# Kernel optimization log

Measured on AMD Instinct MI355X. Metric: run time of the kernel, lower is better.

Reference implementation:

```python
import jax, jax.numpy as jnp
import numpy as np

B, N, D, L, K, H = 64, 576, 768, 64, 5, 8  # batch, tokens, dim, out_token_len, knn k, heads
HD = D // H
SCALE = HD ** -0.5


def layer_norm(x, g, b, eps=1e-5):
    m = jnp.mean(x, axis=-1, keepdims=True)
    v = jnp.mean((x - m) ** 2, axis=-1, keepdims=True)
    return (x - m) * jax.lax.rsqrt(v + eps) * g + b


def cluster(feat, noise):
    # DPC-KNN: pairwise distances, k-NN density, parent distance, peak selection
    sq = jnp.sum(feat * feat, axis=-1)  # [B,N]
    dm = sq[:, :, None] + sq[:, None, :] - 2.0 * jnp.einsum('bnd,bmd->bnm', feat, feat)
    dm = jnp.sqrt(jnp.maximum(dm, 0.0)) / jnp.sqrt(jnp.asarray(D, feat.dtype))  # [B,N,N]
    neg_near, _ = jax.lax.top_k(-dm, K)                       # k smallest distances (negated)
    density = jnp.exp(-jnp.mean(neg_near ** 2, axis=-1))      # [B,N]
    density = density + noise * 1e-6                          # deterministic tie-break
    mask = (density[:, None, :] > density[:, :, None]).astype(feat.dtype)
    dist_max = jnp.max(dm.reshape(dm.shape[0], -1), axis=-1)[:, None, None]
    dist = jnp.min(dm * mask + dist_max * (1.0 - mask), axis=-1)  # [B,N]
    score = dist * density
    _, idx_down = jax.lax.top_k(score, L)                     # [B,L] cluster centers
    dm_down = jnp.take_along_axis(dm, idx_down[:, :, None], axis=1)  # [B,L,N]
    idx_cluster = jnp.argmin(dm_down, axis=1)                 # [B,N] assign to nearest center
    idx_cluster = idx_cluster.at[jnp.arange(dm.shape[0])[:, None], idx_down].set(
        jnp.arange(L)[None, :])
    return idx_cluster


def merger(feat, idx_cluster, token_score):
    b, n, d = feat.shape
    idx = (idx_cluster + jnp.arange(b)[:, None] * L).reshape(-1)       # [B*N]
    tw = jnp.exp(token_score)                                          # [B,N,1]
    all_w = jax.ops.segment_sum(tw.reshape(-1, 1), idx, num_segments=b * L) + 1e-6
    norm_w = tw / all_w[idx].reshape(b, n, 1)
    merged = jax.ops.segment_sum((feat * norm_w).reshape(-1, d), idx, num_segments=b * L)
    return merged.reshape(b, L, d)


def setup_inputs() -> dict:
    key = jax.random.key(0)
    ks = jax.random.split(key, 16)
    s = 0.02
    return {
        'x': jax.random.normal(ks[0], (B, N, D), jnp.float32),
        'density_noise': jax.random.uniform(ks[1], (B, N), jnp.float32),
        'norm1_g': jnp.ones((D,), jnp.float32),
        'norm1_b': jnp.zeros((D,), jnp.float32),
        'score_w': s * jax.random.normal(ks[2], (D, 1), jnp.float32),
        'score_b': jnp.zeros((1,), jnp.float32),
        'wq': s * jax.random.normal(ks[3], (D, D), jnp.float32),
        'wk': s * jax.random.normal(ks[4], (D, D), jnp.float32),
        'wv': s * jax.random.normal(ks[5], (D, D), jnp.float32),
        'proj_w': s * jax.random.normal(ks[6], (D, D), jnp.float32),
        'proj_b': jnp.zeros((D,), jnp.float32),
        'norm2_g': jnp.ones((D,), jnp.float32),
        'norm2_b': jnp.zeros((D,), jnp.float32),
        'fc1_w': s * jax.random.normal(ks[7], (D, 4 * D), jnp.float32),
        'fc1_b': jnp.zeros((4 * D,), jnp.float32),
        'fc2_w': s * jax.random.normal(ks[8], (4 * D, D), jnp.float32),
        'fc2_b': jnp.zeros((D,), jnp.float32),
    }


def reference(x, density_noise, norm1_g, norm1_b, score_w, score_b, wq, wk, wv,
              proj_w, proj_b, norm2_g, norm2_b, fc1_w, fc1_b, fc2_w, fc2_b):
    xn = layer_norm(x, norm1_g, norm1_b)                 # [B,N,D]
    token_score = xn @ score_w + score_b                 # [B,N,1]
    idx_cluster = cluster(jax.lax.stop_gradient(xn), density_noise)  # no-grad in torch
    q_input = merger(xn, idx_cluster, token_score)       # [B,L,D]
    kv = xn
    # STMAttention: cross-attn with token_score bias added to logits
    q = (q_input @ wq).reshape(B, L, H, HD).transpose(0, 2, 1, 3)
    k = (kv @ wk).reshape(B, N, H, HD).transpose(0, 2, 1, 3)
    v = (kv @ wv).reshape(B, N, H, HD).transpose(0, 2, 1, 3)
    dots = jnp.einsum('bhid,bhjd->bhij', q, k) * SCALE   # [B,H,L,N]
    bias = token_score[:, :, 0][:, None, None, :]        # [B,1,1,N]
    attn = jax.nn.softmax(dots + bias, axis=-1)
    out = jnp.einsum('bhij,bhjd->bhid', attn, v)
    out = out.transpose(0, 2, 1, 3).reshape(B, L, D)
    out = out @ proj_w + proj_b
    feature = q_input + out
    h = layer_norm(feature, norm2_g, norm2_b)
    h = jax.nn.gelu(h @ fc1_w + fc1_b, approximate=False) @ fc2_w + fc2_b
    return feature + h
```

## Files before the change

kernel.cpp:

```cpp
#include <hip/hip_runtime.h>
#include <math.h>

#define B_   64
#define N_   576
#define D_   768
#define L_   64
#define H_   8
#define HD_  96
#define NB_  (B_*N_)
#define ML_  (B_*L_)
#define KV_STRIDE_ 1536
#define SCALE_ 0.10206207f
#define INV_SQRT_D_ 0.03608439182f
#define LO_SCALE_ 4.8828125e-4f

typedef __attribute__((ext_vector_type(8))) _Float16 half8v;
typedef __attribute__((ext_vector_type(4))) float floatx4;

__device__ __forceinline__ unsigned short f2h(float f) {
  _Float16 h = (_Float16)f;
  unsigned short u; __builtin_memcpy(&u, &h, 2);
  return u;
}
__device__ __forceinline__ float h2f(unsigned short u) {
  _Float16 h; __builtin_memcpy(&h, &u, 2);
  return (float)h;
}
__device__ __forceinline__ void gload_lds16(const void* g, void* l) {
  __builtin_amdgcn_global_load_lds(
      (const __attribute__((address_space(1))) unsigned*)g,
      (__attribute__((address_space(3))) unsigned*)l, 16, 0, 0);
}

__global__ __launch_bounds__(256) void k_ln1(const float* __restrict__ x,
    const float* __restrict__ g, const float* __restrict__ bt,
    const float* __restrict__ sw, const float* __restrict__ sb,
    unsigned short* __restrict__ xh, unsigned short* __restrict__ xl,
    float* __restrict__ ts, float* __restrict__ sq)
{
  int row = blockIdx.x, tid = threadIdx.x;
  const float* xr = x + (size_t)row * D_;
  float v0 = xr[tid], v1 = xr[tid + 256], v2 = xr[tid + 512];
  __shared__ float r1[256], r2[256];
  r1[tid] = v0 + v1 + v2;
  r2[tid] = v0 * v0 + v1 * v1 + v2 * v2;
  __syncthreads();
  for (int o = 128; o > 0; o >>= 1) {
    if (tid < o) { r1[tid] += r1[tid + o]; r2[tid] += r2[tid + o]; }
    __syncthreads();
  }
  float mean = r1[0] * (1.0f / D_);
  float var  = r2[0] * (1.0f / D_) - mean * mean;
  float rstd = rsqrtf(var + 1e-5f);
  __syncthreads();
  float o0 = (v0 - mean) * rstd * g[tid      ] + bt[tid      ];
  float o1 = (v1 - mean) * rstd * g[tid + 256] + bt[tid + 256];
  float o2 = (v2 - mean) * rstd * g[tid + 512] + bt[tid + 512];
  auto split = [](float o, unsigned short& hu, unsigned short& lu) {
    _Float16 h = (_Float16)o;
    float hf = (float)h;
    _Float16 l = (_Float16)((o - hf) * 2048.0f);
    __builtin_memcpy(&hu, &h, 2);
    __builtin_memcpy(&lu, &l, 2);
  };
  unsigned short h0, l0, h1, l1, h2, l2;
  split(o0, h0, l0); split(o1, h1, l1); split(o2, h2, l2);
  unsigned short* xho = xh + (size_t)row * D_;
  unsigned short* xlo = xl + (size_t)row * D_;
  xho[tid] = h0; xho[tid + 256] = h1; xho[tid + 512] = h2;
  xlo[tid] = l0; xlo[tid + 256] = l1; xlo[tid + 512] = l2;
  r1[tid] = o0 * sw[tid] + o1 * sw[tid + 256] + o2 * sw[tid + 512];
  r2[tid] = o0 * o0 + o1 * o1 + o2 * o2;
  __syncthreads();
  for (int o = 128; o > 0; o >>= 1) {
    if (tid < o) { r1[tid] += r1[tid + o]; r2[tid] += r2[tid + o]; }
    __syncthreads();
  }
  if (tid == 0) { ts[row] = r1[0] + sb[0]; sq[row] = r2[0]; }
}

__global__ __launch_bounds__(256) void k_dmg(const unsigned short* __restrict__ xh,
    const unsigned short* __restrict__ xl, const float* __restrict__ sq,
    float* __restrict__ dm, float* __restrict__ dmax)
{
  __shared__ __align__(16) unsigned short S[4][96 * 64];
  int flat = blockIdx.x;
  int xcd = flat & 7, seq = flat >> 3;
  int b = (seq / 21) * 8 + xcd;
  int t = seq % 21;
  int ti = 0, rl = 6;
  while (t >= rl) { t -= rl; ++ti; --rl; }
  int tj = ti + t;
  int tid = threadIdx.x;
  int wave = tid >> 6, lane = tid & 63;
  int wr = (wave >> 1) * 48, wc = (wave & 1) * 48;
  int mloc = lane & 15, quad = lane >> 4;
  size_t rowA = (size_t)b * N_ + ti * 96;
  size_t rowB = (size_t)b * N_ + tj * 96;

  const unsigned short* srcbase =
      (wave == 0) ? xh + rowA * D_ :
      (wave == 1) ? xl + rowA * D_ :
      (wave == 2) ? xh + rowB * D_ : xl + rowB * D_;
  int lrow = lane >> 3, lchunk = lane & 7;
  const unsigned short* gsrc0 = srcbase + (size_t)lrow * D_ + ((lchunk ^ lrow) * 8);
  unsigned short* lbase = &S[wave][0];

  floatx4 a1[3][3], a2[3][3];
#pragma unroll
  for (int i = 0; i < 3; ++i)
#pragma unroll
    for (int j = 0; j < 3; ++j) {
      a1[i][j] = (floatx4){0.f, 0.f, 0.f, 0.f};
      a2[i][j] = (floatx4){0.f, 0.f, 0.f, 0.f};
    }

  for (int kt = 0; kt < D_; kt += 64) {
    __syncthreads();
#pragma unroll
    for (int rb = 0; rb < 12; ++rb)
      gload_lds16(gsrc0 + (size_t)rb * 8 * D_ + kt, lbase + rb * 8 * 64);
    __syncthreads();
#pragma unroll
    for (int ks = 0; ks < 2; ++ks) {
      half8v ah[3], al[3], bh[3], bl[3];
      int cperm = (((ks << 2) | quad) ^ (mloc & 7)) * 8;
#pragma unroll
      for (int i = 0; i < 3; ++i) {
        int ro = (wr + i * 16 + mloc) * 64 + cperm;
        ah[i] = *(const half8v*)&S[0][ro];
        al[i] = *(const half8v*)&S[1][ro];
      }
#pragma unroll
      for (int j = 0; j < 3; ++j) {
        int ro = (wc + j * 16 + mloc) * 64 + cperm;
        bh[j] = *(const half8v*)&S[2][ro];
        bl[j] = *(const half8v*)&S[3][ro];
      }
#pragma unroll
      for (int i = 0; i < 3; ++i)
#pragma unroll
        for (int j = 0; j < 3; ++j) {
          a1[i][j] = __builtin_amdgcn_mfma_f32_16x16x32_f16(ah[i], bh[j], a1[i][j], 0, 0, 0);
          a2[i][j] = __builtin_amdgcn_mfma_f32_16x16x32_f16(ah[i], bl[j], a2[i][j], 0, 0, 0);
          a2[i][j] = __builtin_amdgcn_mfma_f32_16x16x32_f16(al[i], bh[j], a2[i][j], 0, 0, 0);
        }
    }
  }

  const float* sqb = sq + b * N_;
  float* dmb = dm + (size_t)b * N_ * N_;
  bool diag = (ti == tj);
  float vmax = 0.f;
#pragma unroll
  for (int j = 0; j < 3; ++j) {
    int gj = tj * 96 + wc + j * 16 + mloc;
    float sj = sqb[gj];
#pragma unroll
    for (int i = 0; i < 3; ++i) {
      int gi0 = ti * 96 + wr + i * 16 + quad * 4;
#pragma unroll
      for (int reg = 0; reg < 4; ++reg) {
        int gi = gi0 + reg;
        float g = a1[i][j][reg] + a2[i][j][reg] * LO_SCALE_;
        float d = sqb[gi] + sj - 2.0f * g;
        float v = sqrtf(fmaxf(d, 0.0f)) * INV_SQRT_D_;
        vmax = fmaxf(vmax, v);
        if (!diag || gj >= gi) {
          dmb[(size_t)gi * N_ + gj] = v;
          dmb[(size_t)gj * N_ + gi] = v;
        }
      }
    }
  }
#pragma unroll
  for (int msk = 32; msk >= 1; msk >>= 1) vmax = fmaxf(vmax, __shfl_xor(vmax, msk));
  if (lane == 0) atomicMax((unsigned int*)(dmax + b), __float_as_uint(vmax));
}

__global__ __launch_bounds__(64) void k_density(const float* __restrict__ dm,
    const float* __restrict__ noise, float* __restrict__ den)
{
  int row = blockIdx.x, lane = threadIdx.x;
  const float* r = dm + (size_t)row * N_;
  float a0 = 1e30f, a1 = 1e30f, a2 = 1e30f, a3 = 1e30f, a4 = 1e30f;
  auto ins5 = [&](float xv) {
    a4 = fminf(a4, xv);
    float t;
    t = fminf(a3, a4); a4 = fmaxf(a3, a4); a3 = t;
    t = fminf(a2, a3); a3 = fmaxf(a2, a3); a2 = t;
    t = fminf(a1, a2); a2 = fmaxf(a1, a2); a1 = t;
    t = fminf(a0, a1); a1 = fmaxf(a0, a1); a0 = t;
  };
#pragma unroll
  for (int t = 0; t < 9; ++t) ins5(r[lane + 64 * t]);
  for (int m = 1; m < 64; m <<= 1) {
    float b0 = __shfl_xor(a0, m), b1 = __shfl_xor(a1, m), b2 = __shfl_xor(a2, m);
    float b3 = __shfl_xor(a3, m), b4 = __shfl_xor(a4, m);
    ins5(b0); ins5(b1); ins5(b2); ins5(b3); ins5(b4);
  }
  if (lane == 0) {
    float ms = (a0 * a0 + a1 * a1 + a2 * a2 + a3 * a3 + a4 * a4) * 0.2f;
    den[row] = expf(-ms) + noise[row] * 1e-6f;
  }
}

__global__ __launch_bounds__(64) void k_dist(const float* __restrict__ dm,
    const float* __restrict__ den, const float* __restrict__ dmax,
    float* __restrict__ score)
{
  int row = blockIdx.x, lane = threadIdx.x;
  int b = row / N_;
  float di = den[row], dx = dmax[b];
  const float* r = dm + (size_t)row * N_;
  const float* db = den + b * N_;
  float m = dx;
#pragma unroll
  for (int t = 0; t < 9; ++t) {
    int j = lane + 64 * t;
    float v = (db[j] > di) ? r[j] : dx;
    m = fminf(m, v);
  }
  for (int msk = 1; msk < 64; msk <<= 1) m = fminf(m, __shfl_xor(m, msk));
  if (lane == 0) score[row] = m * di;
}

__global__ __launch_bounds__(256) void k_topL(const float* __restrict__ score,
    int* __restrict__ idxd)
{
  int b = blockIdx.x, tid = threadIdx.x;
  __shared__ float s[1024];
  __shared__ int   si[1024];
  for (int i = tid; i < 1024; i += 256) {
    s[i] = (i < N_) ? score[b * N_ + i] : -3.0e38f;
    si[i] = i;
  }
  __syncthreads();
  for (int k = 2; k <= 1024; k <<= 1) {
    for (int j = k >> 1; j > 0; j >>= 1) {
#pragma unroll
      for (int t = 0; t < 2; ++t) {
        int idx512 = tid + t * 256;
        int lo = idx512 & (j - 1);
        int i = ((idx512 ^ lo) << 1) | lo;
        int p = i | j;
        float as = s[i], bs = s[p];
        int ai = si[i], bi = si[p];
        bool bba = (bs > as) || (bs == as && bi < ai);
        bool up = ((i & k) == 0);
        bool dosw = up ? bba : !bba;
        if (dosw) { s[i] = bs; s[p] = as; si[i] = bi; si[p] = ai; }
      }
      __syncthreads();
    }
  }
  if (tid < L_) idxd[b * L_ + tid] = si[tid];
}

__global__ __launch_bounds__(576) void k_assign(const float* __restrict__ dm,
    const int* __restrict__ idxd, int* __restrict__ idxc)
{
  int b = blockIdx.x, n = threadIdx.x;
  __shared__ int ctr[L_];
  if (n < L_) ctr[n] = idxd[b * L_ + n];
  __syncthreads();
  const float* dmb = dm + (size_t)b * N_ * N_;
  float best = 1e30f; int bl = 0;
  for (int l = 0; l < L_; ++l) {
    float v = dmb[(size_t)ctr[l] * N_ + n];
    if (v < best) { best = v; bl = l; }
  }
  for (int l = 0; l < L_; ++l)
    if (ctr[l] == n) bl = l;
  idxc[b * N_ + n] = bl;
}

__global__ __launch_bounds__(64) void k_bucket(const int* __restrict__ idxc,
    int* __restrict__ ord, int* __restrict__ starts)
{
  int b = blockIdx.x, l = threadIdx.x;
  __shared__ int ic[N_];
  for (int n = l; n < N_; n += 64) ic[n] = idxc[b * N_ + n];
  __syncthreads();
  int cnt = 0;
  for (int n = 0; n < N_; ++n) cnt += (ic[n] == l) ? 1 : 0;
  int inc = cnt;
  for (int d = 1; d < 64; d <<= 1) {
    int v = __shfl_up(inc, d);
    if (l >= d) inc += v;
  }
  int excl = inc - cnt;
  if (l == 0) starts[b * 65] = 0;
  starts[b * 65 + l + 1] = inc;
  int p = excl;
  for (int n = 0; n < N_; ++n)
    if (ic[n] == l) ord[b * N_ + p++] = n;
}

__global__ __launch_bounds__(256) void k_merge(const unsigned short* __restrict__ xh,
    const unsigned short* __restrict__ xl,
    const float* __restrict__ ts, const int* __restrict__ ord,
    const int* __restrict__ starts, float* __restrict__ qin)
{
  int blk = blockIdx.x;
  int b = blk >> 6, l = blk & 63;
  int tid = threadIdx.x;
  int s0 = starts[b * 65 + l], s1 = starts[b * 65 + l + 1];
  const float* tsb = ts + b * N_;
  const int* ob = ord + b * N_;
  const unsigned short* xhb = xh + (size_t)b * N_ * D_;
  const unsigned short* xlb = xl + (size_t)b * N_ * D_;
  float a0 = 0.f, a1 = 0.f, a2 = 0.f, wsum = 0.f;
  for (int k = s0; k < s1; ++k) {
    int n = ob[k];
    float w = expf(tsb[n]);
    wsum += w;
    const unsigned short* hr = xhb + (size_t)n * D_;
    const unsigned short* lr = xlb + (size_t)n * D_;
    float x0 = h2f(hr[tid      ]) + h2f(lr[tid      ]) * LO_SCALE_;
    float x1 = h2f(hr[tid + 256]) + h2f(lr[tid + 256]) * LO_SCALE_;
    float x2 = h2f(hr[tid + 512]) + h2f(lr[tid + 512]) * LO_SCALE_;
    a0 += w * x0; a1 += w * x1; a2 += w * x2;
  }
  float inv = 1.0f / (wsum + 1e-6f);
  float* q = qin + (size_t)blk * D_;
  q[tid] = a0 * inv; q[tid + 256] = a1 * inv; q[tid + 512] = a2 * inv;
}

__global__ __launch_bounds__(256) void k_wt(const float* __restrict__ W,
    unsigned short* __restrict__ WT, int K, int N)
{
  __shared__ float t[32][33];
  int k0 = blockIdx.x * 32, n0 = blockIdx.y * 32;
  int tid = threadIdx.x;
  int r = tid >> 3, c4 = (tid & 7) * 4;
  float4 v = *(const float4*)(W + (size_t)(k0 + r) * N + n0 + c4);
  t[r][c4] = v.x; t[r][c4 + 1] = v.y; t[r][c4 + 2] = v.z; t[r][c4 + 3] = v.w;
  __syncthreads();
  ushort4 s4;
  s4.x = f2h(t[c4 + 0][r]); s4.y = f2h(t[c4 + 1][r]);
  s4.z = f2h(t[c4 + 2][r]); s4.w = f2h(t[c4 + 3][r]);
  *(ushort4*)(WT + (size_t)(n0 + r) * K + k0 + c4) = s4;
}

template<int EPI, int ASRC>
__global__ __launch_bounds__(256) void k_mgemm(const void* __restrict__ Ap_,
    const unsigned short* __restrict__ Wt, const float* __restrict__ bias,
    const float* __restrict__ res, void* __restrict__ outp,
    int M, int Nd, int Kd)
{
  __shared__ __align__(16) unsigned short As[128 * 64];
  __shared__ __align__(16) unsigned short Bs[128 * 64];
  int tid = threadIdx.x;
  int gn = Nd >> 7;
  int flat = blockIdx.x;
  int xcd = flat & 7, seq = flat >> 3;
  int bmg = seq / gn, bnn = seq - bmg * gn;
  int bm = (bmg * 8 + xcd) * 128, bn = bnn * 128;
  int wave = tid >> 6, lane = tid & 63;
  int wr = (wave >> 1) * 64, wc = (wave & 1) * 64;
  int mloc = lane & 15, quad = lane >> 4;

  floatx4 acc[4][4];
#pragma unroll
  for (int i = 0; i < 4; ++i)
#pragma unroll
    for (int j = 0; j < 4; ++j)
      acc[i][j] = (floatx4){0.f, 0.f, 0.f, 0.f};

  int lrow = lane >> 3, lchunk = lane & 7;
  const unsigned short* bsrc0 =
      Wt + (size_t)(bn + wave * 32 + lrow) * Kd + ((lchunk ^ lrow) * 8);
  unsigned short* bdst0 = &Bs[(wave * 32) * 64];
  const unsigned short* asrc0 = (ASRC == 1)
      ? (const unsigned short*)Ap_ + (size_t)(bm + wave * 32 + lrow) * Kd + ((lchunk ^ lrow) * 8)
      : nullptr;
  unsigned short* adst0 = &As[(wave * 32) * 64];

  for (int kt = 0; kt < Kd; kt += 64) {
    __syncthreads();
#pragma unroll
    for (int rb = 0; rb < 4; ++rb)
      gload_lds16(bsrc0 + (size_t)rb * 8 * Kd + kt, bdst0 + rb * 8 * 64);
    if (ASRC == 1) {
#pragma unroll
      for (int rb = 0; rb < 4; ++rb)
        gload_lds16(asrc0 + (size_t)rb * 8 * Kd + kt, adst0 + rb * 8 * 64);
    } else {
      const float* A = (const float*)Ap_;
#pragma unroll
      for (int it = 0; it < 4; ++it) {
        int idx = tid + it * 256;
        int r = idx >> 3, c = idx & 7;
        const float* ap = A + (size_t)(bm + r) * Kd + kt + c * 8;
        float4 f0 = *(const float4*)ap;
        float4 f1 = *(const float4*)(ap + 4);
        uint4 pk;
        pk.x = (unsigned)f2h(f0.x) | ((unsigned)f2h(f0.y) << 16);
        pk.y = (unsigned)f2h(f0.z) | ((unsigned)f2h(f0.w) << 16);
        pk.z = (unsigned)f2h(f1.x) | ((unsigned)f2h(f1.y) << 16);
        pk.w = (unsigned)f2h(f1.z) | ((unsigned)f2h(f1.w) << 16);
        *(uint4*)&As[r * 64 + ((c ^ (r & 7)) * 8)] = pk;
      }
    }
    __syncthreads();
#pragma unroll
    for (int ks = 0; ks < 2; ++ks) {
      half8v af[4], bf[4];
      int cperm = (((ks << 2) | quad) ^ (mloc & 7)) * 8;
#pragma unroll
      for (int i = 0; i < 4; ++i)
        af[i] = *(const half8v*)&As[(wr + i * 16 + mloc) * 64 + cperm];
#pragma unroll
      for (int j = 0; j < 4; ++j)
        bf[j] = *(const half8v*)&Bs[(wc + j * 16 + mloc) * 64 + cperm];
#pragma unroll
      for (int i = 0; i < 4; ++i)
#pragma unroll
        for (int j = 0; j < 4; ++j)
          acc[i][j] = __builtin_amdgcn_mfma_f32_16x16x32_f16(af[i], bf[j], acc[i][j], 0, 0, 0);
    }
  }

  float bv[4] = {0.f, 0.f, 0.f, 0.f};
  if (EPI >= 1) {
#pragma unroll
    for (int j = 0; j < 4; ++j) bv[j] = bias[bn + wc + j * 16 + mloc];
  }
#pragma unroll
  for (int i = 0; i < 4; ++i) {
    int gr0 = bm + wr + i * 16 + quad * 4;
#pragma unroll
    for (int j = 0; j < 4; ++j) {
      int gcn = bn + wc + j * 16 + mloc;
#pragma unroll
      for (int reg = 0; reg < 4; ++reg) {
        float v = acc[i][j][reg];
        size_t off = (size_t)(gr0 + reg) * Nd + gcn;
        if (EPI == 0) {
          ((unsigned short*)outp)[off] = f2h(v);
        } else if (EPI == 1) {
          ((float*)outp)[off] = v + bv[j] + res[off];
        } else {
          v += bv[j];
          v = 0.5f * v * (1.0f + erff(v * 0.70710678f));
          ((unsigned short*)outp)[off] = f2h(v);
        }
      }
    }
  }
}

__global__ __launch_bounds__(256) void k_attn(const unsigned short* __restrict__ Qu,
    const unsigned short* __restrict__ KVu, const float* __restrict__ ts,
    float* __restrict__ aout)
{
  __shared__ __align__(16) unsigned short Ks[64 * 104];
  __shared__ __align__(16) unsigned short VsT[96 * 64];
  __shared__ __align__(16) unsigned short sPa[64 * 64];
  __shared__ float tsb[64];
  int h = blockIdx.x, b = blockIdx.y;
  int tid = threadIdx.x;
  int wave = tid >> 6, lane = tid & 63;
  int mloc = lane & 15, quad = lane >> 4;

  half8v qf[3];
  {
    const unsigned short* qrow = Qu + (size_t)(b * 64 + wave * 16 + mloc) * D_ + h * 96 + quad * 8;
#pragma unroll
    for (int k = 0; k < 3; ++k) qf[k] = *(const half8v*)(qrow + k * 32);
  }

  floatx4 of[6];
#pragma unroll
  for (int dt = 0; dt < 6; ++dt) of[dt] = (floatx4){0.f, 0.f, 0.f, 0.f};
  float m[4], l[4];
#pragma unroll
  for (int r = 0; r < 4; ++r) { m[r] = -1e30f; l[r] = 0.f; }

  for (int jt = 0; jt < 9; ++jt) {
    int j0 = jt * 64;
    __syncthreads();
#pragma unroll
    for (int t = 0; t < 3; ++t) {
      int id = tid + t * 256;
      int row = id / 12, c = id % 12;
      *(uint4*)&Ks[row * 104 + c * 8] =
          *(const uint4*)(KVu + (size_t)(b * N_ + j0 + row) * KV_STRIDE_ + h * 96 + c * 8);
    }
#pragma unroll
    for (int t = 0; t < 3; ++t) {
      int id = tid + t * 256;
      int keyp = id & 31, dq = (id >> 5) * 4;
      int key = keyp * 2;
      const unsigned short* vp =
          KVu + (size_t)(b * N_ + j0 + key) * KV_STRIDE_ + 768 + h * 96 + dq;
      ushort4 v0 = *(const ushort4*)vp;
      ushort4 v1 = *(const ushort4*)(vp + KV_STRIDE_);
      unsigned pk0 = (unsigned)v0.x | ((unsigned)v1.x << 16);
      unsigned pk1 = (unsigned)v0.y | ((unsigned)v1.y << 16);
      unsigned pk2 = (unsigned)v0.z | ((unsigned)v1.z << 16);
      unsigned pk3 = (unsigned)v0.w | ((unsigned)v1.w << 16);
      int cbase = key >> 3, off = key & 7;
#pragma unroll
      for (int i = 0; i < 4; ++i) {
        int d = dq + i;
        unsigned pv = (i == 0) ? pk0 : (i == 1) ? pk1 : (i == 2) ? pk2 : pk3;
        *(unsigned*)&VsT[d * 64 + ((cbase ^ (d & 7)) << 3) + off] = pv;
      }
    }
    if (tid < 64) tsb[tid] = ts[b * N_ + j0 + tid];
    __syncthreads();

    floatx4 acc[4];
#pragma unroll
    for (int j = 0; j < 4; ++j) acc[j] = (floatx4){0.f, 0.f, 0.f, 0.f};
#pragma unroll
    for (int j = 0; j < 4; ++j)
#pragma unroll
      for (int k = 0; k < 3; ++k) {
        half8v kf = *(const half8v*)&Ks[(j * 16 + mloc) * 104 + k * 32 + quad * 8];
        acc[j] = __builtin_amdgcn_mfma_f32_16x16x32_f16(qf[k], kf, acc[j], 0, 0, 0);
      }

    float ts4[4];
#pragma unroll
    for (int j = 0; j < 4; ++j) ts4[j] = tsb[j * 16 + mloc];
    float rm[4] = {-1e30f, -1e30f, -1e30f, -1e30f};
#pragma unroll
    for (int j = 0; j < 4; ++j)
#pragma unroll
      for (int r = 0; r < 4; ++r) {
        acc[j][r] = acc[j][r] * SCALE_ + ts4[j];
        rm[r] = fmaxf(rm[r], acc[j][r]);
      }
#pragma unroll
    for (int r = 0; r < 4; ++r) {
      rm[r] = fmaxf(rm[r], __shfl_xor(rm[r], 1));
      rm[r] = fmaxf(rm[r], __shfl_xor(rm[r], 2));
      rm[r] = fmaxf(rm[r], __shfl_xor(rm[r], 4));
      rm[r] = fmaxf(rm[r], __shfl_xor(rm[r], 8));
    }
    float alpha[4], rs[4];
#pragma unroll
    for (int r = 0; r < 4; ++r) {
      float mn = fmaxf(m[r], rm[r]);
      alpha[r] = __expf(m[r] - mn);
      m[r] = mn;
      rs[r] = 0.f;
    }
#pragma unroll
    for (int j = 0; j < 4; ++j)
#pragma unroll
      for (int r = 0; r < 4; ++r) {
        float p = __expf(acc[j][r] - m[r]);
        acc[j][r] = p; rs[r] += p;
      }
#pragma unroll
    for (int r = 0; r < 4; ++r) {
      rs[r] += __shfl_xor(rs[r], 1); rs[r] += __shfl_xor(rs[r], 2);
      rs[r] += __shfl_xor(rs[r], 4); rs[r] += __shfl_xor(rs[r], 8);
      l[r] = l[r] * alpha[r] + rs[r];
    }
#pragma unroll
    for (int dt = 0; dt < 6; ++dt)
#pragma unroll
      for (int r = 0; r < 4; ++r) of[dt][r] *= alpha[r];

#pragma unroll
    for (int j = 0; j < 4; ++j)
#pragma unroll
      for (int r = 0; r < 4; ++r) {
        int row = wave * 16 + quad * 4 + r;
        int key = j * 16 + mloc;
        sPa[row * 64 + (((key >> 3) ^ (row & 7)) << 3) + (key & 7)] = f2h(acc[j][r]);
      }
    half8v pa[2];
    int prow = wave * 16 + mloc;
#pragma unroll
    for (int f2 = 0; f2 < 2; ++f2)
      pa[f2] = *(const half8v*)&sPa[prow * 64 + (((f2 * 4 + quad) ^ (prow & 7)) << 3)];
#pragma unroll
    for (int dt = 0; dt < 6; ++dt)
#pragma unroll
      for (int f2 = 0; f2 < 2; ++f2) {
        int vrow = dt * 16 + mloc;
        half8v vf = *(const half8v*)&VsT[vrow * 64 + (((f2 * 4 + quad) ^ (vrow & 7)) << 3)];
        of[dt] = __builtin_amdgcn_mfma_f32_16x16x32_f16(pa[f2], vf, of[dt], 0, 0, 0);
      }
  }

  float linv[4];
#pragma unroll
  for (int r = 0; r < 4; ++r) linv[r] = 1.0f / l[r];
#pragma unroll
  for (int dt = 0; dt < 6; ++dt)
#pragma unroll
    for (int r = 0; r < 4; ++r) {
      int row = b * 64 + wave * 16 + quad * 4 + r;
      int col = h * 96 + dt * 16 + mloc;
      aout[(size_t)row * D_ + col] = of[dt][r] * linv[r];
    }
}

__global__ __launch_bounds__(256) void k_ln2(const float* __restrict__ f,
    const float* __restrict__ g, const float* __restrict__ bt, float* __restrict__ out)
{
  int row = blockIdx.x, tid = threadIdx.x;
  const float* fr = f + (size_t)row * D_;
  float v0 = fr[tid], v1 = fr[tid + 256], v2 = fr[tid + 512];
  __shared__ float r1[256], r2[256];
  r1[tid] = v0 + v1 + v2;
  r2[tid] = v0 * v0 + v1 * v1 + v2 * v2;
  __syncthreads();
  for (int o = 128; o > 0; o >>= 1) {
    if (tid < o) { r1[tid] += r1[tid + o]; r2[tid] += r2[tid + o]; }
    __syncthreads();
  }
  float mean = r1[0] * (1.0f / D_);
  float var  = r2[0] * (1.0f / D_) - mean * mean;
  float rstd = rsqrtf(var + 1e-5f);
  float* oo = out + (size_t)row * D_;
  oo[tid      ] = (v0 - mean) * rstd * g[tid      ] + bt[tid      ];
  oo[tid + 256] = (v1 - mean) * rstd * g[tid + 256] + bt[tid + 256];
  oo[tid + 512] = (v2 - mean) * rstd * g[tid + 512] + bt[tid + 512];
}

extern "C" void kernel_launch(void* const* d_in, const int* in_sizes, int n_in,
                              void* d_out, int out_size, void* d_ws, size_t ws_size,
                              hipStream_t stream)
{
  (void)in_sizes; (void)n_in; (void)out_size; (void)ws_size;
  const float* x    = (const float*)d_in[0];
  const float* nois = (const float*)d_in[1];
  const float* n1g  = (const float*)d_in[2];
  const float* n1b  = (const float*)d_in[3];
  const float* sw   = (const float*)d_in[4];
  const float* sb   = (const float*)d_in[5];
  const float* wq   = (const float*)d_in[6];
  const float* wk   = (const float*)d_in[7];
  const float* wv   = (const float*)d_in[8];
  const float* pw   = (const float*)d_in[9];
  const float* pb   = (const float*)d_in[10];
  const float* n2g  = (const float*)d_in[11];
  const float* n2b  = (const float*)d_in[12];
  const float* f1w  = (const float*)d_in[13];
  const float* f1b  = (const float*)d_in[14];
  const float* f2w  = (const float*)d_in[15];
  const float* f2b  = (const float*)d_in[16];

  float* ws    = (float*)d_ws;
  unsigned short* XH = (unsigned short*)ws;
  unsigned short* XL = XH + (size_t)NB_ * D_;
  float* RG    = ws + (size_t)NB_ * D_;
  float* QIN   = RG + (size_t)NB_ * D_;
  float* FEAT  = QIN + (size_t)ML_ * D_;
  float* AOUT  = FEAT + (size_t)ML_ * D_;
  float* QBUF  = AOUT + (size_t)ML_ * D_;
  float* P     = QBUF + (size_t)ML_ * D_;
  unsigned short* QH16 = (unsigned short*)P;  P += (size_t)ML_ * D_ / 2;
  unsigned short* WTQ  = (unsigned short*)P;  P += (size_t)D_ * D_ / 2;
  unsigned short* WTKV = (unsigned short*)P;  P += (size_t)D_ * D_;
  unsigned short* WTP  = (unsigned short*)P;  P += (size_t)D_ * D_ / 2;
  unsigned short* WT1  = (unsigned short*)P;  P += (size_t)D_ * 4 * D_ / 2;
  unsigned short* WT2  = (unsigned short*)P;  P += (size_t)D_ * 4 * D_ / 2;
  float* TS    = P;
  float* SQ    = TS + NB_;
  float* DEN   = SQ + NB_;
  float* SCORE = DEN + NB_;
  float* DMAX  = SCORE + NB_;
  int*   IDXD  = (int*)(DMAX + 64);
  int*   IDXC  = IDXD + ML_;
  int*   ORD   = IDXC + NB_;
  int*   STARTS= ORD + NB_;
  float* DM    = RG;
  unsigned short* KVB = (unsigned short*)RG;
  unsigned short* HID = (unsigned short*)RG;

  hipMemsetAsync(DMAX, 0, 64 * sizeof(float), stream);
  k_wt<<<dim3(24, 24), 256, 0, stream>>>(wq, WTQ, D_, D_);
  k_wt<<<dim3(24, 24), 256, 0, stream>>>(wk, WTKV, D_, D_);
  k_wt<<<dim3(24, 24), 256, 0, stream>>>(wv, WTKV + (size_t)D_ * D_, D_, D_);
  k_wt<<<dim3(24, 24), 256, 0, stream>>>(pw, WTP, D_, D_);
  k_wt<<<dim3(24, 96), 256, 0, stream>>>(f1w, WT1, D_, 4 * D_);
  k_wt<<<dim3(96, 24), 256, 0, stream>>>(f2w, WT2, 4 * D_, D_);

  k_ln1<<<NB_, 256, 0, stream>>>(x, n1g, n1b, sw, sb, XH, XL, TS, SQ);
  k_dmg<<<1344, 256, 0, stream>>>(XH, XL, SQ, DM, DMAX);
  k_density<<<NB_, 64, 0, stream>>>(DM, nois, DEN);
  k_dist<<<NB_, 64, 0, stream>>>(DM, DEN, DMAX, SCORE);
  k_topL<<<B_, 256, 0, stream>>>(SCORE, IDXD);
  k_assign<<<B_, 576, 0, stream>>>(DM, IDXD, IDXC);
  k_bucket<<<B_, 64, 0, stream>>>(IDXC, ORD, STARTS);
  k_merge<<<ML_, 256, 0, stream>>>(XH, XL, TS, ORD, STARTS, QIN);

  k_mgemm<0, 0><<<(ML_ / 128) * (D_ / 128), 256, 0, stream>>>(
      QIN, WTQ, nullptr, nullptr, QH16, ML_, D_, D_);
  k_mgemm<0, 1><<<(NB_ / 128) * (KV_STRIDE_ / 128), 256, 0, stream>>>(
      XH, WTKV, nullptr, nullptr, KVB, NB_, KV_STRIDE_, D_);
  k_attn<<<dim3(H_, B_), 256, 0, stream>>>(QH16, KVB, TS, AOUT);
  k_mgemm<1, 0><<<(ML_ / 128) * (D_ / 128), 256, 0, stream>>>(
      AOUT, WTP, pb, QIN, FEAT, ML_, D_, D_);
  k_ln2<<<ML_, 256, 0, stream>>>(FEAT, n2g, n2b, QBUF);
  k_mgemm<2, 0><<<(ML_ / 128) * ((4 * D_) / 128), 256, 0, stream>>>(
      QBUF, WT1, f1b, nullptr, HID, ML_, 4 * D_, D_);
  k_mgemm<1, 1><<<(ML_ / 128) * (D_ / 128), 256, 0, stream>>>(
      HID, WT2, f2b, FEAT, d_out, ML_, D_, 4 * D_);
}
```

Measured before the change: 815.8 us.

## Fuse cluster stages and weight transposes, vectorize density/dist row scans

Merges top-L selection, nearest-center assignment and bucketing into a single per-batch kernel that keeps centers and assignments in shared memory, and folds the six weight-transpose launches into one flat launch. The density and distance kernels now process four rows per 256-thread block and read rows with float4 loads. This cuts kernel launch count and global round-trips for the intermediate index arrays, at the cost of a 576-thread block where most threads sit idle during the bitonic sort and bucketing phases.

```diff
diff --git a/kernel.cpp b/kernel.cpp
--- a/kernel.cpp
+++ b/kernel.cpp
@@ -178,10 +178,11 @@
   if (lane == 0) atomicMax((unsigned int*)(dmax + b), __float_as_uint(vmax));
 }
 
-__global__ __launch_bounds__(64) void k_density(const float* __restrict__ dm,
+__global__ __launch_bounds__(256) void k_density(const float* __restrict__ dm,
     const float* __restrict__ noise, float* __restrict__ den)
 {
-  int row = blockIdx.x, lane = threadIdx.x;
+  int row = blockIdx.x * 4 + (threadIdx.x >> 6);
+  int lane = threadIdx.x & 63;
   const float* r = dm + (size_t)row * N_;
   float a0 = 1e30f, a1 = 1e30f, a2 = 1e30f, a3 = 1e30f, a4 = 1e30f;
   auto ins5 = [&](float xv) {
@@ -192,8 +193,14 @@
     t = fminf(a1, a2); a2 = fmaxf(a1, a2); a1 = t;
     t = fminf(a0, a1); a1 = fmaxf(a0, a1); a0 = t;
   };
-#pragma unroll
-  for (int t = 0; t < 9; ++t) ins5(r[lane + 64 * t]);
+  float4 v0 = *(const float4*)(r + lane * 4);
+  float4 v1 = *(const float4*)(r + (lane + 64) * 4);
+  ins5(v0.x); ins5(v0.y); ins5(v0.z); ins5(v0.w);
+  ins5(v1.x); ins5(v1.y); ins5(v1.z); ins5(v1.w);
+  if (lane < 16) {
+    float4 v2 = *(const float4*)(r + (lane + 128) * 4);
+    ins5(v2.x); ins5(v2.y); ins5(v2.z); ins5(v2.w);
+  }
   for (int m = 1; m < 64; m <<= 1) {
     float b0 = __shfl_xor(a0, m), b1 = __shfl_xor(a1, m), b2 = __shfl_xor(a2, m);
     float b3 = __shfl_xor(a3, m), b4 = __shfl_xor(a4, m);
@@ -205,44 +212,49 @@
   }
 }
 
-__global__ __launch_bounds__(64) void k_dist(const float* __restrict__ dm,
+__global__ __launch_bounds__(256) void k_dist(const float* __restrict__ dm,
     const float* __restrict__ den, const float* __restrict__ dmax,
     float* __restrict__ score)
 {
-  int row = blockIdx.x, lane = threadIdx.x;
+  int row = blockIdx.x * 4 + (threadIdx.x >> 6);
+  int lane = threadIdx.x & 63;
   int b = row / N_;
   float di = den[row], dx = dmax[b];
   const float* r = dm + (size_t)row * N_;
   const float* db = den + b * N_;
   float m = dx;
-#pragma unroll
-  for (int t = 0; t < 9; ++t) {
-    int j = lane + 64 * t;
-    float v = (db[j] > di) ? r[j] : dx;
-    m = fminf(m, v);
-  }
+  auto proc4 = [&](int f4) {
+    float4 rv = *(const float4*)(r + f4 * 4);
+    float4 dv = *(const float4*)(db + f4 * 4);
+    m = fminf(m, (dv.x > di) ? rv.x : dx);
+    m = fminf(m, (dv.y > di) ? rv.y : dx);
+    m = fminf(m, (dv.z > di) ? rv.z : dx);
+    m = fminf(m, (dv.w > di) ? rv.w : dx);
+  };
+  proc4(lane); proc4(lane + 64);
+  if (lane < 16) proc4(lane + 128);
   for (int msk = 1; msk < 64; msk <<= 1) m = fminf(m, __shfl_xor(m, msk));
   if (lane == 0) score[row] = m * di;
 }
 
-__global__ __launch_bounds__(256) void k_topL(const float* __restrict__ score,
-    int* __restrict__ idxd)
+__global__ __launch_bounds__(576) void k_cluster(const float* __restrict__ score,
+    const float* __restrict__ dm, int* __restrict__ ord, int* __restrict__ starts)
 {
   int b = blockIdx.x, tid = threadIdx.x;
   __shared__ float s[1024];
   __shared__ int   si[1024];
-  for (int i = tid; i < 1024; i += 256) {
+  __shared__ int   ctr[L_];
+  __shared__ int   icS[N_];
+  for (int i = tid; i < 1024; i += 576) {
     s[i] = (i < N_) ? score[b * N_ + i] : -3.0e38f;
     si[i] = i;
   }
   __syncthreads();
   for (int k = 2; k <= 1024; k <<= 1) {
     for (int j = k >> 1; j > 0; j >>= 1) {
-#pragma unroll
-      for (int t = 0; t < 2; ++t) {
-        int idx512 = tid + t * 256;
-        int lo = idx512 & (j - 1);
-        int i = ((idx512 ^ lo) << 1) | lo;
+      if (tid < 512) {
+        int lo = tid & (j - 1);
+        int i = ((tid ^ lo) << 1) | lo;
         int p = i | j;
         float as = s[i], bs = s[p];
         int ai = si[i], bi = si[p];
@@ -254,47 +266,37 @@
       __syncthreads();
     }
   }
-  if (tid < L_) idxd[b * L_ + tid] = si[tid];
-}
-
-__global__ __launch_bounds__(576) void k_assign(const float* __restrict__ dm,
-    const int* __restrict__ idxd, int* __restrict__ idxc)
-{
-  int b = blockIdx.x, n = threadIdx.x;
-  __shared__ int ctr[L_];
-  if (n < L_) ctr[n] = idxd[b * L_ + n];
+  if (tid < L_) ctr[tid] = si[tid];
   __syncthreads();
-  const float* dmb = dm + (size_t)b * N_ * N_;
-  float best = 1e30f; int bl = 0;
-  for (int l = 0; l < L_; ++l) {
-    float v = dmb[(size_t)ctr[l] * N_ + n];
-    if (v < best) { best = v; bl = l; }
-  }
-  for (int l = 0; l < L_; ++l)
-    if (ctr[l] == n) bl = l;
-  idxc[b * N_ + n] = bl;
-}
-
-__global__ __launch_bounds__(64) void k_bucket(const int* __restrict__ idxc,
-    int* __restrict__ ord, int* __restrict__ starts)
-{
-  int b = blockIdx.x, l = threadIdx.x;
-  __shared__ int ic[N_];
-  for (int n = l; n < N_; n += 64) ic[n] = idxc[b * N_ + n];
+  {
+    int n = tid;
+    const float* dmb = dm + (size_t)b * N_ * N_;
+    float best = 1e30f; int bl = 0;
+    for (int l = 0; l < L_; ++l) {
+      float v = dmb[(size_t)ctr[l] * N_ + n];
+      if (v < best) { best = v; bl = l; }
+    }
+    for (int l = 0; l < L_; ++l)
+      if (ctr[l] == n) bl = l;
+    icS[n] = bl;
+  }
   __syncthreads();
-  int cnt = 0;
-  for (int n = 0; n < N_; ++n) cnt += (ic[n] == l) ? 1 : 0;
-  int inc = cnt;
-  for (int d = 1; d < 64; d <<= 1) {
-    int v = __shfl_up(inc, d);
-    if (l >= d) inc += v;
-  }
-  int excl = inc - cnt;
-  if (l == 0) starts[b * 65] = 0;
-  starts[b * 65 + l + 1] = inc;
-  int p = excl;
-  for (int n = 0; n < N_; ++n)
-    if (ic[n] == l) ord[b * N_ + p++] = n;
+  if (tid < L_) {
+    int l = tid;
+    int cnt = 0;
+    for (int nn = 0; nn < N_; ++nn) cnt += (icS[nn] == l) ? 1 : 0;
+    int inc = cnt;
+    for (int d = 1; d < 64; d <<= 1) {
+      int v = __shfl_up(inc, d);
+      if (l >= d) inc += v;
+    }
+    int excl = inc - cnt;
+    if (l == 0) starts[b * 65] = 0;
+    starts[b * 65 + l + 1] = inc;
+    int p = excl;
+    for (int nn = 0; nn < N_; ++nn)
+      if (icS[nn] == l) ord[b * N_ + p++] = nn;
+  }
 }
 
 __global__ __launch_bounds__(256) void k_merge(const unsigned short* __restrict__ xh,
@@ -327,11 +329,31 @@
   q[tid] = a0 * inv; q[tid + 256] = a1 * inv; q[tid + 512] = a2 * inv;
 }
 
-__global__ __launch_bounds__(256) void k_wt(const float* __restrict__ W,
-    unsigned short* __restrict__ WT, int K, int N)
+__global__ __launch_bounds__(256) void k_wt6(
+    const float* __restrict__ wq, const float* __restrict__ wk,
+    const float* __restrict__ wv, const float* __restrict__ pw,
+    const float* __restrict__ f1w, const float* __restrict__ f2w,
+    unsigned short* __restrict__ WTQ, unsigned short* __restrict__ WTKV,
+    unsigned short* __restrict__ WTP, unsigned short* __restrict__ WT1,
+    unsigned short* __restrict__ WT2)
 {
   __shared__ float t[32][33];
-  int k0 = blockIdx.x * 32, n0 = blockIdx.y * 32;
+  int flat = blockIdx.x;
+  const float* W; unsigned short* WT; int K, N, kx, ny;
+  if (flat < 2304) {
+    int wi = flat / 576, tt = flat % 576;
+    K = D_; N = D_; kx = tt % 24; ny = tt / 24;
+    W  = (wi == 0) ? wq : (wi == 1) ? wk : (wi == 2) ? wv : pw;
+    WT = (wi == 0) ? WTQ : (wi == 1) ? WTKV
+       : (wi == 2) ? (WTKV + (size_t)D_ * D_) : WTP;
+  } else if (flat < 4608) {
+    int tt = flat - 2304; K = D_; N = 4 * D_; kx = tt % 24; ny = tt / 24;
+    W = f1w; WT = WT1;
+  } else {
+    int tt = flat - 4608; K = 4 * D_; N = D_; kx = tt % 96; ny = tt / 96;
+    W = f2w; WT = WT2;
+  }
+  int k0 = kx * 32, n0 = ny * 32;
   int tid = threadIdx.x;
   int r = tid >> 3, c4 = (tid & 7) * 4;
   float4 v = *(const float4*)(W + (size_t)(k0 + r) * N + n0 + c4);
@@ -678,20 +700,14 @@
   unsigned short* HID = (unsigned short*)RG;
 
   hipMemsetAsync(DMAX, 0, 64 * sizeof(float), stream);
-  k_wt<<<dim3(24, 24), 256, 0, stream>>>(wq, WTQ, D_, D_);
-  k_wt<<<dim3(24, 24), 256, 0, stream>>>(wk, WTKV, D_, D_);
-  k_wt<<<dim3(24, 24), 256, 0, stream>>>(wv, WTKV + (size_t)D_ * D_, D_, D_);
-  k_wt<<<dim3(24, 24), 256, 0, stream>>>(pw, WTP, D_, D_);
-  k_wt<<<dim3(24, 96), 256, 0, stream>>>(f1w, WT1, D_, 4 * D_);
-  k_wt<<<dim3(96, 24), 256, 0, stream>>>(f2w, WT2, 4 * D_, D_);
+  k_wt6<<<6912, 256, 0, stream>>>(wq, wk, wv, pw, f1w, f2w,
+                                  WTQ, WTKV, WTP, WT1, WT2);
 
   k_ln1<<<NB_, 256, 0, stream>>>(x, n1g, n1b, sw, sb, XH, XL, TS, SQ);
   k_dmg<<<1344, 256, 0, stream>>>(XH, XL, SQ, DM, DMAX);
-  k_density<<<NB_, 64, 0, stream>>>(DM, nois, DEN);
-  k_dist<<<NB_, 64, 0, stream>>>(DM, DEN, DMAX, SCORE);
-  k_topL<<<B_, 256, 0, stream>>>(SCORE, IDXD);
-  k_assign<<<B_, 576, 0, stream>>>(DM, IDXD, IDXC);
-  k_bucket<<<B_, 64, 0, stream>>>(IDXC, ORD, STARTS);
+  k_density<<<NB_ / 4, 256, 0, stream>>>(DM, nois, DEN);
+  k_dist<<<NB_ / 4, 256, 0, stream>>>(DM, DEN, DMAX, SCORE);
+  k_cluster<<<B_, 576, 0, stream>>>(SCORE, DM, ORD, STARTS);
   k_merge<<<ML_, 256, 0, stream>>>(XH, XL, TS, ORD, STARTS, QIN);
 
   k_mgemm<0, 0><<<(ML_ / 128) * (D_ / 128), 256, 0, stream>>>(
```

Result: no change. 819.7 us (+0.5%).
